# Performance work log

Measured on AMD Instinct MI355X. Metric: run time of the kernel, lower is better.

The kernel has to match this reference:

```python
import jax, jax.numpy as jnp
import numpy as np

N_EMB = 512
DIM = 64
BETA = 0.25
EPS = 1e-10


def setup_inputs() -> dict:
    key = jax.random.key(0)
    k1, k2 = jax.random.split(key)
    z = jax.random.normal(k1, (32, 64, 64, 64), dtype=jnp.float32)  # (B, C=DIM, H, W)
    # embedding weight initialized uniform(-1/K, 1/K) as in the module
    weight = jax.random.uniform(k2, (N_EMB, DIM), dtype=jnp.float32,
                                minval=-1.0 / N_EMB, maxval=1.0 / N_EMB)
    return {"z": z, "weight": weight}


def reference(z, weight):
    # (B,C,H,W) -> (B,H,W,C)
    zp = jnp.transpose(z, (0, 2, 3, 1))
    zf = zp.reshape(-1, DIM)  # (N, D)
    # pairwise squared distances ||z||^2 + ||e||^2 - 2 z.e  -> (N, K)
    d = (jnp.sum(zf * zf, axis=1, keepdims=True)
         + jnp.sum(weight * weight, axis=1)
         - 2.0 * zf @ weight.T)
    codebook = jnp.argmin(d, axis=1)  # (N,)
    encodings = jax.nn.one_hot(codebook, N_EMB, dtype=zf.dtype)  # (N, K)
    # direct gather == one_hot @ weight (same math, efficient form)
    z_q = weight[codebook].reshape(zp.shape)
    sg = jax.lax.stop_gradient
    loss = jnp.mean((sg(z_q) - zp) ** 2) + BETA * jnp.mean((z_q - sg(zp)) ** 2)
    # straight-through estimator
    z_q = zp + sg(z_q - zp)
    e_mean = jnp.mean(encodings, axis=0)
    perplexity = jnp.exp(-jnp.sum(e_mean * jnp.log(e_mean + EPS)))
    z_q = jnp.transpose(z_q, (0, 3, 1, 2))  # back to (B,C,H,W)
    return (loss, z_q, perplexity, encodings, codebook)
```

## Files before the change

### kernel.cpp

```cpp
#include <hip/hip_runtime.h>
#include <math.h>

#define NK 512
#define NPTS (32*64*64)
#define NELEM (32*64*64*64)

typedef float nvf4 __attribute__((ext_vector_type(4)));

#define OFF_LOSS 0
#define OFF_ZQ   1
#define OFF_PERP (1 + NELEM)
#define OFF_ENC  (2 + NELEM)
#define OFF_CB   (2 + NELEM + (size_t)NPTS * NK)


__global__ __launch_bounds__(256) void vq_prep(const float* __restrict__ wg,
                                               float* __restrict__ wT,
                                               float* __restrict__ bnd) {
    __shared__ float tl[64 * 65];
    const int t = threadIdx.x;
    const int kbase = blockIdx.x * 64;
    #pragma unroll
    for (int it = 0; it < 16; ++it) {
        int i = it * 256 + t;
        int k = i >> 6, d = i & 63;
        tl[k * 65 + d] = wg[(size_t)(kbase + k) * 64 + d];
    }
    __syncthreads();
    #pragma unroll
    for (int it = 0; it < 16; ++it) {
        int j = it * 256 + t;
        int d = j >> 6, kk = j & 63;
        wT[(size_t)d * 512 + kbase + kk] = tl[kk * 65 + d];
    }
    if (t < 64) {
        float s = 0.f;
        #pragma unroll 4
        for (int d = 0; d < 64; ++d) {
            float v = tl[t * 65 + d];
            s = __fadd_rn(s, __fmul_rn(v, v));
        }
        bnd[kbase + t] = s;
    }
}

__global__ __launch_bounds__(256) void vq_main(const float* __restrict__ zg,
                                               const float* __restrict__ wg,
                                               const float* __restrict__ wT,
                                               const float* __restrict__ bndg,
                                               float* __restrict__ out,
                                               int* __restrict__ hist,
                                               double* __restrict__ lossAcc) {
    const int t = threadIdx.x;
    const int blk = blockIdx.x;
    const int b = blk >> 6;
    const int h = blk & 63;

    __shared__ __align__(16) float zt[64 * 64];
    __shared__ __align__(16) float wt[64 * 128];
    __shared__ float aRow[64];
    __shared__ int   idxs[64];
    __shared__ float wsum[4];

    float* zqt  = wt;
    float* redv = wt + 4096;
    int*   redi = (int*)(wt + 4096 + 16 * 68);

    const float4* wT4 = (const float4*)wT;
    float4* wt4 = (float4*)wt;
    const int d0 = t >> 5, c4 = t & 31;

    float4 pf[8];
    #pragma unroll
    for (int s = 0; s < 8; ++s)
        pf[s] = wT4[(size_t)(d0 + s * 8) * 128 + c4];

    {
        const int w = t & 63;
        const int c0 = t >> 6;
        const size_t base = (size_t)b * 262144 + (size_t)h * 64;
        #pragma unroll
        for (int c = c0; c < 64; c += 4)
            zt[c * 64 + w] = zg[base + (size_t)c * 4096 + w];
    }
    __syncthreads();

    if (t < 64) {
        float s = 0.f;
        for (int d = 0; d < 64; ++d) {
            float v = zt[d * 64 + t];
            s = __fadd_rn(s, __fmul_rn(v, v));
        }
        aRow[t] = s;
    }
    __syncthreads();

    const int tx = t & 15;
    const int ty = t >> 4;
    const int p0 = tx * 4;
    const int ty8 = ty * 8;

    float av[4];
    #pragma unroll
    for (int i = 0; i < 4; ++i) av[i] = aRow[p0 + i];

    float best[4];
    int bidx[4];
    #pragma unroll
    for (int i = 0; i < 4; ++i) { best[i] = INFINITY; bidx[i] = 0; }

    for (int c = 0; c < 4; ++c) {
        if (c) __syncthreads();

        #pragma unroll
        for (int s = 0; s < 8; ++s)
            wt4[(d0 + s * 8) * 32 + c4] = pf[s];

        if (c < 3) {
            #pragma unroll
            for (int s = 0; s < 8; ++s)
                pf[s] = wT4[(size_t)(d0 + s * 8) * 128 + (c + 1) * 32 + c4];
        }

        float bn[8];
        {
            const float4* bp = (const float4*)(bndg + c * 128 + ty8);
            float4 b0 = bp[0], b1 = bp[1];
            bn[0] = b0.x; bn[1] = b0.y; bn[2] = b0.z; bn[3] = b0.w;
            bn[4] = b1.x; bn[5] = b1.y; bn[6] = b1.z; bn[7] = b1.w;
        }
        __syncthreads();

        float acc[4][8];
        #pragma unroll
        for (int i = 0; i < 4; ++i)
            #pragma unroll
            for (int j = 0; j < 8; ++j) acc[i][j] = 0.f;

        const float* ztp = zt + p0;
        const float* wtp = wt + ty8;
        #pragma unroll 4
        for (int d = 0; d < 64; ++d) {
            const float4 zv = *(const float4*)(ztp + d * 64);
            const float4 w0 = *(const float4*)(wtp + d * 128);
            const float4 w1 = *(const float4*)(wtp + d * 128 + 4);
            const float zr[4] = {zv.x, zv.y, zv.z, zv.w};
            const float wr[8] = {w0.x, w0.y, w0.z, w0.w, w1.x, w1.y, w1.z, w1.w};
            #pragma unroll
            for (int i = 0; i < 4; ++i)
                #pragma unroll
                for (int j = 0; j < 8; ++j)
                    acc[i][j] = fmaf(zr[i], wr[j], acc[i][j]);
        }

        #pragma unroll
        for (int i = 0; i < 4; ++i) {
            #pragma unroll
            for (int j = 0; j < 8; ++j) {
                float dist = __fsub_rn(__fadd_rn(av[i], bn[j]), 2.0f * acc[i][j]);
                int k = c * 128 + ty8 + j;
                if (dist < best[i]) { best[i] = dist; bidx[i] = k; }
            }
        }
    }
    __syncthreads();

    #pragma unroll
    for (int i = 0; i < 4; ++i) {
        redv[ty * 68 + p0 + i] = best[i];
        redi[ty * 64 + p0 + i] = bidx[i];
    }
    __syncthreads();

    if (t < 64) {
        float bv = redv[t];
        int bi = redi[t];
        #pragma unroll
        for (int x = 1; x < 16; ++x) {
            float v = redv[x * 68 + t];
            int ii = redi[x * 64 + t];
            if (v < bv || (v == bv && ii < bi)) { bv = v; bi = ii; }
        }
        idxs[t] = bi;
        atomicAdd(&hist[bi], 1);
        out[OFF_CB + (size_t)blk * 64 + t] = (float)bi;
        const float4* wr4 = (const float4*)(wg + (size_t)bi * 64);
        #pragma unroll
        for (int q = 0; q < 16; ++q) {
            float4 v = wr4[q];
            zqt[(4 * q + 0) * 64 + t] = v.x;
            zqt[(4 * q + 1) * 64 + t] = v.y;
            zqt[(4 * q + 2) * 64 + t] = v.z;
            zqt[(4 * q + 3) * 64 + t] = v.w;
        }
    }
    __syncthreads();

    {
        nvf4* enc = (nvf4*)(out + OFF_ENC + (size_t)blk * 64 * NK);
        #pragma unroll
        for (int it = 0; it < 32; ++it) {
            int e = it * 256 + t;
            int r = e >> 7, cc = e & 127;
            int idx = idxs[r];
            nvf4 v = (nvf4)(0.f);
            if ((idx >> 2) == cc) v[idx & 3] = 1.0f;
            __builtin_nontemporal_store(v, &enc[(size_t)r * 128 + cc]);
        }
    }

    float lsum = 0.f;
    {
        float* zq = out + OFF_ZQ + (size_t)b * 262144 + (size_t)h * 64;
        #pragma unroll
        for (int it = 0; it < 4; ++it) {
            int f = it * 256 + t;
            int d = f >> 4, pp = (f & 15) * 4;
            float4 zv = *(const float4*)(zt + d * 64 + pp);
            float4 qv = *(const float4*)(zqt + d * 64 + pp);
            nvf4 o;
            float dx = __fsub_rn(qv.x, zv.x); lsum = __fadd_rn(lsum, __fmul_rn(dx, dx)); o[0] = __fadd_rn(zv.x, dx);
            float dy = __fsub_rn(qv.y, zv.y); lsum = __fadd_rn(lsum, __fmul_rn(dy, dy)); o[1] = __fadd_rn(zv.y, dy);
            float dz = __fsub_rn(qv.z, zv.z); lsum = __fadd_rn(lsum, __fmul_rn(dz, dz)); o[2] = __fadd_rn(zv.z, dz);
            float dw = __fsub_rn(qv.w, zv.w); lsum = __fadd_rn(lsum, __fmul_rn(dw, dw)); o[3] = __fadd_rn(zv.w, dw);
            __builtin_nontemporal_store(o, (nvf4*)(zq + (size_t)d * 4096 + pp));
        }
    }
    #pragma unroll
    for (int off = 32; off > 0; off >>= 1)
        lsum += __shfl_down(lsum, off);
    if ((t & 63) == 0) wsum[t >> 6] = lsum;
    __syncthreads();
    if (t == 0) {
        float tot = (wsum[0] + wsum[1]) + (wsum[2] + wsum[3]);
        atomicAdd(lossAcc, (double)tot);
    }
}

__global__ __launch_bounds__(512) void vq_finalize(const int* __restrict__ hist,
                                                   const double* __restrict__ lossAcc,
                                                   float* __restrict__ out) {
    __shared__ float sh[512];
    const int t = threadIdx.x;
    float p = (float)hist[t] / (float)NPTS;
    sh[t] = __fmul_rn(p, logf(__fadd_rn(p, 1e-10f)));
    __syncthreads();
    for (int s = 256; s > 0; s >>= 1) {
        if (t < s) sh[t] += sh[t + s];
        __syncthreads();
    }
    if (t == 0) {
        float m = (float)(*lossAcc / (double)NELEM);
        out[OFF_LOSS] = __fadd_rn(m, __fmul_rn(0.25f, m));
        out[OFF_PERP] = expf(-sh[0]);
    }
}

extern "C" void kernel_launch(void* const* d_in, const int* in_sizes, int n_in,
                              void* d_out, int out_size, void* d_ws, size_t ws_size,
                              hipStream_t stream) {
    const float* z = (const float*)d_in[0];
    const float* w = (const float*)d_in[1];
    float* out = (float*)d_out;
    int* hist = (int*)d_ws;
    double* lossAcc = (double*)((char*)d_ws + 2048);
    float* wT = (float*)((char*)d_ws + 4096);
    float* bnd = wT + 64 * 512;

    (void)hipMemsetAsync(d_ws, 0, 4096, stream);
    vq_prep<<<8, 256, 0, stream>>>(w, wT, bnd);
    vq_main<<<2048, 256, 0, stream>>>(z, w, wT, bnd, out, hist, lossAcc);
    vq_finalize<<<1, 512, 0, stream>>>(hist, lossAcc, out);
}
```

Before: 467.8 us.

## Enlarge distance tile to 8x8 per thread with 256-code chunks, drop prefetch

Reworks the main distance GEMM so each thread computes an 8x8 tile over 256-code chunks, taking two passes instead of four. This raises arithmetic intensity per shared-memory load. It also drops the register prefetch of the next weight chunk in favour of a direct global-to-shared copy, and sets launch bounds to two blocks per SM. The encodings and z_q outputs now use plain stores instead of nontemporal ones. The larger shared buffer (64 KB) and higher register use may reduce occupancy, and losing the prefetch exposes load latency.

```diff
diff --git a/kernel.cpp b/kernel.cpp
--- a/kernel.cpp
+++ b/kernel.cpp
@@ -4,8 +4,6 @@
 #define NK 512
 #define NPTS (32*64*64)
 #define NELEM (32*64*64*64)
-
-typedef float nvf4 __attribute__((ext_vector_type(4)));
 
 #define OFF_LOSS 0
 #define OFF_ZQ   1
@@ -44,36 +42,27 @@
     }
 }
 
-__global__ __launch_bounds__(256) void vq_main(const float* __restrict__ zg,
-                                               const float* __restrict__ wg,
-                                               const float* __restrict__ wT,
-                                               const float* __restrict__ bndg,
-                                               float* __restrict__ out,
-                                               int* __restrict__ hist,
-                                               double* __restrict__ lossAcc) {
+__global__ __launch_bounds__(256, 2) void vq_main(const float* __restrict__ zg,
+                                                  const float* __restrict__ wg,
+                                                  const float* __restrict__ wT,
+                                                  const float* __restrict__ bndg,
+                                                  float* __restrict__ out,
+                                                  int* __restrict__ hist,
+                                                  double* __restrict__ lossAcc) {
     const int t = threadIdx.x;
     const int blk = blockIdx.x;
     const int b = blk >> 6;
     const int h = blk & 63;
 
     __shared__ __align__(16) float zt[64 * 64];
-    __shared__ __align__(16) float wt[64 * 128];
-    __shared__ float aRow[64];
-    __shared__ int   idxs[64];
-    __shared__ float wsum[4];
-
-    float* zqt  = wt;
-    float* redv = wt + 4096;
-    int*   redi = (int*)(wt + 4096 + 16 * 68);
-
-    const float4* wT4 = (const float4*)wT;
-    float4* wt4 = (float4*)wt;
-    const int d0 = t >> 5, c4 = t & 31;
-
-    float4 pf[8];
-    #pragma unroll
-    for (int s = 0; s < 8; ++s)
-        pf[s] = wT4[(size_t)(d0 + s * 8) * 128 + c4];
+    __shared__ __align__(16) float wt[64 * 256];
+
+    float* aRow = wt;
+    float* redv = wt;
+    int*   redi = (int*)(wt + 2048);
+    float* zqt  = wt + 4096;
+    int*   idxs = (int*)(wt + 8192);
+    float* wsum = wt + 8256;
 
     {
         const int w = t & 63;
@@ -95,70 +84,76 @@
     }
     __syncthreads();
 
-    const int tx = t & 15;
-    const int ty = t >> 4;
-    const int p0 = tx * 4;
-    const int ty8 = ty * 8;
-
-    float av[4];
-    #pragma unroll
-    for (int i = 0; i < 4; ++i) av[i] = aRow[p0 + i];
-
-    float best[4];
-    int bidx[4];
-    #pragma unroll
-    for (int i = 0; i < 4; ++i) { best[i] = INFINITY; bidx[i] = 0; }
-
-    for (int c = 0; c < 4; ++c) {
+    const int tx = t & 7;
+    const int ty = t >> 3;
+    const int p0 = tx * 8;
+    const int k0 = ty * 8;
+
+    float av[8];
+    {
+        float4 a0 = *(const float4*)(aRow + p0);
+        float4 a1 = *(const float4*)(aRow + p0 + 4);
+        av[0] = a0.x; av[1] = a0.y; av[2] = a0.z; av[3] = a0.w;
+        av[4] = a1.x; av[5] = a1.y; av[6] = a1.z; av[7] = a1.w;
+    }
+    __syncthreads();
+
+    float best[8];
+    int bidx[8];
+    #pragma unroll
+    for (int i = 0; i < 8; ++i) { best[i] = INFINITY; bidx[i] = 0; }
+
+    const float4* wT4 = (const float4*)wT;
+    float4* wt4 = (float4*)wt;
+
+    for (int c = 0; c < 2; ++c) {
         if (c) __syncthreads();
 
         #pragma unroll
-        for (int s = 0; s < 8; ++s)
-            wt4[(d0 + s * 8) * 32 + c4] = pf[s];
-
-        if (c < 3) {
-            #pragma unroll
-            for (int s = 0; s < 8; ++s)
-                pf[s] = wT4[(size_t)(d0 + s * 8) * 128 + (c + 1) * 32 + c4];
+        for (int it = 0; it < 16; ++it) {
+            int i = it * 256 + t;
+            int d = i >> 6, c4 = i & 63;
+            wt4[d * 64 + c4] = wT4[(size_t)d * 128 + c * 64 + c4];
         }
 
         float bn[8];
         {
-            const float4* bp = (const float4*)(bndg + c * 128 + ty8);
+            const float4* bp = (const float4*)(bndg + c * 256 + k0);
             float4 b0 = bp[0], b1 = bp[1];
             bn[0] = b0.x; bn[1] = b0.y; bn[2] = b0.z; bn[3] = b0.w;
             bn[4] = b1.x; bn[5] = b1.y; bn[6] = b1.z; bn[7] = b1.w;
         }
         __syncthreads();
 
-        float acc[4][8];
-        #pragma unroll
-        for (int i = 0; i < 4; ++i)
+        float acc[8][8];
+        #pragma unroll
+        for (int i = 0; i < 8; ++i)
             #pragma unroll
             for (int j = 0; j < 8; ++j) acc[i][j] = 0.f;
 
         const float* ztp = zt + p0;
-        const float* wtp = wt + ty8;
+        const float* wtp = wt + k0;
         #pragma unroll 4
         for (int d = 0; d < 64; ++d) {
-            const float4 zv = *(const float4*)(ztp + d * 64);
-            const float4 w0 = *(const float4*)(wtp + d * 128);
-            const float4 w1 = *(const float4*)(wtp + d * 128 + 4);
-            const float zr[4] = {zv.x, zv.y, zv.z, zv.w};
+            float4 z0 = *(const float4*)(ztp + d * 64);
+            float4 z1 = *(const float4*)(ztp + d * 64 + 4);
+            float4 w0 = *(const float4*)(wtp + d * 256);
+            float4 w1 = *(const float4*)(wtp + d * 256 + 4);
+            const float zr[8] = {z0.x, z0.y, z0.z, z0.w, z1.x, z1.y, z1.z, z1.w};
             const float wr[8] = {w0.x, w0.y, w0.z, w0.w, w1.x, w1.y, w1.z, w1.w};
             #pragma unroll
-            for (int i = 0; i < 4; ++i)
+            for (int i = 0; i < 8; ++i)
                 #pragma unroll
                 for (int j = 0; j < 8; ++j)
                     acc[i][j] = fmaf(zr[i], wr[j], acc[i][j]);
         }
 
         #pragma unroll
-        for (int i = 0; i < 4; ++i) {
+        for (int i = 0; i < 8; ++i) {
             #pragma unroll
             for (int j = 0; j < 8; ++j) {
                 float dist = __fsub_rn(__fadd_rn(av[i], bn[j]), 2.0f * acc[i][j]);
-                int k = c * 128 + ty8 + j;
+                int k = c * 256 + k0 + j;
                 if (dist < best[i]) { best[i] = dist; bidx[i] = k; }
             }
         }
@@ -166,8 +161,8 @@
     __syncthreads();
 
     #pragma unroll
-    for (int i = 0; i < 4; ++i) {
-        redv[ty * 68 + p0 + i] = best[i];
+    for (int i = 0; i < 8; ++i) {
+        redv[ty * 64 + p0 + i] = best[i];
         redi[ty * 64 + p0 + i] = bidx[i];
     }
     __syncthreads();
@@ -176,8 +171,8 @@
         float bv = redv[t];
         int bi = redi[t];
         #pragma unroll
-        for (int x = 1; x < 16; ++x) {
-            float v = redv[x * 68 + t];
+        for (int x = 1; x < 32; ++x) {
+            float v = redv[x * 64 + t];
             int ii = redi[x * 64 + t];
             if (v < bv || (v == bv && ii < bi)) { bv = v; bi = ii; }
         }
@@ -197,15 +192,15 @@
     __syncthreads();
 
     {
-        nvf4* enc = (nvf4*)(out + OFF_ENC + (size_t)blk * 64 * NK);
+        float4* enc = (float4*)(out + OFF_ENC + (size_t)blk * 64 * NK);
         #pragma unroll
         for (int it = 0; it < 32; ++it) {
             int e = it * 256 + t;
             int r = e >> 7, cc = e & 127;
             int idx = idxs[r];
-            nvf4 v = (nvf4)(0.f);
-            if ((idx >> 2) == cc) v[idx & 3] = 1.0f;
-            __builtin_nontemporal_store(v, &enc[(size_t)r * 128 + cc]);
+            float4 v = make_float4(0.f, 0.f, 0.f, 0.f);
+            if ((idx >> 2) == cc) ((float*)&v)[idx & 3] = 1.0f;
+            enc[(size_t)r * 128 + cc] = v;
         }
     }
 
@@ -218,12 +213,12 @@
             int d = f >> 4, pp = (f & 15) * 4;
             float4 zv = *(const float4*)(zt + d * 64 + pp);
             float4 qv = *(const float4*)(zqt + d * 64 + pp);
-            nvf4 o;
-            float dx = __fsub_rn(qv.x, zv.x); lsum = __fadd_rn(lsum, __fmul_rn(dx, dx)); o[0] = __fadd_rn(zv.x, dx);
-            float dy = __fsub_rn(qv.y, zv.y); lsum = __fadd_rn(lsum, __fmul_rn(dy, dy)); o[1] = __fadd_rn(zv.y, dy);
-            float dz = __fsub_rn(qv.z, zv.z); lsum = __fadd_rn(lsum, __fmul_rn(dz, dz)); o[2] = __fadd_rn(zv.z, dz);
-            float dw = __fsub_rn(qv.w, zv.w); lsum = __fadd_rn(lsum, __fmul_rn(dw, dw)); o[3] = __fadd_rn(zv.w, dw);
-            __builtin_nontemporal_store(o, (nvf4*)(zq + (size_t)d * 4096 + pp));
+            float4 o;
+            float dx = __fsub_rn(qv.x, zv.x); lsum = __fadd_rn(lsum, __fmul_rn(dx, dx)); o.x = __fadd_rn(zv.x, dx);
+            float dy = __fsub_rn(qv.y, zv.y); lsum = __fadd_rn(lsum, __fmul_rn(dy, dy)); o.y = __fadd_rn(zv.y, dy);
+            float dz = __fsub_rn(qv.z, zv.z); lsum = __fadd_rn(lsum, __fmul_rn(dz, dz)); o.z = __fadd_rn(zv.z, dz);
+            float dw = __fsub_rn(qv.w, zv.w); lsum = __fadd_rn(lsum, __fmul_rn(dw, dw)); o.w = __fadd_rn(zv.w, dw);
+            *(float4*)(zq + (size_t)d * 4096 + pp) = o;
         }
     }
     #pragma unroll
```

After: 460.7 us. No clear change (-1.5%).
